# Kernel tuning notes

Hardware: AMD Instinct MI355X
Metric: run time of the kernel (lower is better)

## Reference

```python
import jax, jax.numpy as jnp
import numpy as np

HIDDEN = 4096
MAX_STROKES = 1000
INPUT = 5


def setup_inputs() -> dict:
    key = jax.random.key(0)
    ks = jax.random.split(key, 7)
    s = 1.0 / np.sqrt(HIDDEN)  # torch LSTMCell init scale
    return {
        "W_ih": jax.random.normal(ks[0], (4 * HIDDEN, INPUT), jnp.float32) * s,
        "W_hh": jax.random.normal(ks[1], (4 * HIDDEN, HIDDEN), jnp.float32) * s,
        "b_ih": jax.random.normal(ks[2], (4 * HIDDEN,), jnp.float32) * s,
        "b_hh": jax.random.normal(ks[3], (4 * HIDDEN,), jnp.float32) * s,
        "W_lin": jax.random.normal(ks[4], (7, HIDDEN), jnp.float32) * s,
        "b_lin": jax.random.normal(ks[5], (7,), jnp.float32) * s,
        "noise": jax.random.normal(ks[6], (MAX_STROKES, 2), jnp.float32),
    }


def reference(W_ih, W_hh, b_ih, b_hh, W_lin, b_lin, noise):
    # carried state, so h = c = 0 every step; W_hh @ h vanishes.
    init = jnp.array([0.0, 0.0, 1.0, 0.0, 0.0], dtype=W_ih.dtype)
    mu_idx = jnp.array([0, 2])
    lv_idx = jnp.array([1, 3])

    def step(carry, n_t):
        prev, active = carry  # prev: [5], active: bool (loop condition on prev)
        gates = W_ih @ prev + b_ih + b_hh  # [4H]; W_hh @ 0 omitted
        i_g, f_g, g_g, o_g = jnp.split(gates, 4)
        c = jax.nn.sigmoid(i_g) * jnp.tanh(g_g)
        h = jax.nn.sigmoid(o_g) * jnp.tanh(c)
        logits = jnp.tanh(W_lin @ h + b_lin)  # [7]
        pen = jax.nn.softmax(logits[4:])  # [3]
        xy = logits[mu_idx] + jnp.exp(logits[lv_idx] / 2.0) * n_t  # reparam sample
        new_row = jnp.concatenate([xy, pen])  # [5]
        row_out = jnp.where(active, new_row, 0.0)
        next_prev = jnp.where(active, new_row, prev)
        next_active = jnp.logical_and(active, jnp.argmax(new_row[2:]) != 2)
        return (next_prev, next_active), row_out

    (_, _), rows = jax.lax.scan(step, (init, jnp.array(True)), noise)
    return jnp.concatenate([init[None, :], rows], axis=0)  # [MAX_STROKES+1, 5]
```

## Files before the change

kernel.cpp:

```cpp
#include <hip/hip_runtime.h>
#include <math.h>

#define H 4096
#define NSTEPS 1000
#define NT 512
#define NGATEBLK 12
#define NWLBLK 7
#define NREPACK (NGATEBLK + NWLBLK)
#define MAGIC 0x5A17C0DEull

typedef float f32x2 __attribute__((ext_vector_type(2)));


__device__ __forceinline__ unsigned short f2bf(float f) {
    unsigned u = __builtin_bit_cast(unsigned, f);
    u += 0x7FFFu + ((u >> 16) & 1u);
    return (unsigned short)(u >> 16);
}
__device__ __forceinline__ float bf2f(unsigned h) {
    unsigned u = h << 16;
    return __builtin_bit_cast(float, u);
}
__device__ __forceinline__ unsigned long long pack4(float a, float b, float c, float d) {
    return (unsigned long long)f2bf(a) | ((unsigned long long)f2bf(b) << 16)
         | ((unsigned long long)f2bf(c) << 32) | ((unsigned long long)f2bf(d) << 48);
}
__device__ __forceinline__ unsigned pack2(float a, float b) {
    return (unsigned)f2bf(a) | ((unsigned)f2bf(b) << 16);
}

__device__ __forceinline__ f32x2 sig3(f32x2 z) {
    f32x2 z2 = z * z;
    f32x2 p = z2 * (-1.0f / 48.0f) + 0.25f;
    return z * p + 0.5f;
}
__device__ __forceinline__ f32x2 tanh7(f32x2 z) {
    f32x2 z2 = z * z;
    f32x2 p = z2 * (-0.0539682540f) + 0.1333333333f;
    p = z2 * p + (-0.3333333333f);
    return (z * z2) * p + z;
}
__device__ __forceinline__ f32x2 tanh3(f32x2 z) {
    f32x2 z2 = z * z;
    f32x2 p = z2 * (-0.3333333333f) + 1.0f;
    return z * p;
}
__device__ __forceinline__ float poly_tanh(float z) {
    float z2 = z * z;
    float p = fmaf(z2, -0.0539682540f, 0.1333333333f);
    p = fmaf(z2, p, -0.3333333333f);
    return fmaf(z * z2, p, z);
}
__device__ __forceinline__ float poly_exp(float z) {
    float p = fmaf(z, 0.0083333333f, 0.0416666667f);
    p = fmaf(z, p, 0.1666666667f);
    p = fmaf(z, p, 0.5f);
    p = fmaf(z, p, 1.0f);
    return fmaf(z, p, 1.0f);
}

__global__ __launch_bounds__(NT, 1) void sketch_fused(
    const float* __restrict__ W_ih,
    const float* __restrict__ b_ih,
    const float* __restrict__ b_hh,
    const float* __restrict__ W_lin,
    const float* __restrict__ b_lin,
    const float* __restrict__ noise,
    float* __restrict__ out,
    unsigned char* __restrict__ ws)
{
    unsigned long long* ws8 = (unsigned long long*)ws;
    unsigned* wsu = (unsigned*)(ws + (size_t)38 * 512 * 8);
    unsigned long long* flags = (unsigned long long*)(ws + (512u << 10));
    const int tid = threadIdx.x;
    const int blk = blockIdx.x;

    if (blk < NREPACK) {
        if (blk < NGATEBLK) {
            const int g = blk >> 2, p = blk & 3;
            const int up = p * 512 + tid;
            const int s  = up >> 2;
            const int j  = up & 3;
            const size_t f2w = (g == 0) ? 0 : (g == 1 ? (size_t)5 * H : (size_t)15 * H / 2);
            const float2* Wf2 = (const float2*)W_ih;
            float2 A  = Wf2[f2w + 5 * (size_t)up + 0];
            float2 Bv = Wf2[f2w + 5 * (size_t)up + 1];
            float2 Cc = Wf2[f2w + 5 * (size_t)up + 2];
            float2 D  = Wf2[f2w + 5 * (size_t)up + 3];
            float2 E  = Wf2[f2w + 5 * (size_t)up + 4];
            const size_t f2b = (g == 0) ? 0 : (g == 1 ? (size_t)H : (size_t)3 * H / 2);
            float2 bi = ((const float2*)b_ih)[f2b + up];
            float2 bh = ((const float2*)b_hh)[f2b + up];
            float b0 = bi.x + bh.x + Cc.x;
            float b1 = bi.y + bh.y + E.y;
            unsigned long long wA = pack4(A.x, Cc.y, A.y, D.x);
            unsigned long long wB = pack4(Bv.x - Cc.x, D.y - E.y, Bv.y - Cc.x, E.x - E.y);
            const int rA = g * 8 + 2 * j;
            __hip_atomic_store(&ws8[(size_t)rA * 512 + s],       wA, __ATOMIC_RELAXED, __HIP_MEMORY_SCOPE_AGENT);
            __hip_atomic_store(&ws8[(size_t)(rA + 1) * 512 + s], wB, __ATOMIC_RELAXED, __HIP_MEMORY_SCOPE_AGENT);
            __hip_atomic_store(&wsu[(size_t)(g * 4 + j) * 512 + s], pack2(b0, b1),
                               __ATOMIC_RELAXED, __HIP_MEMORY_SCOPE_AGENT);
        } else {
            const int l = blk - NGATEBLK;
            const float4* p4 = (const float4*)(W_lin + (size_t)l * H);
            float4 v0 = p4[2 * tid], v1 = p4[2 * tid + 1];
            unsigned long long wA = pack4(v0.x, v0.y, v0.z, v0.w);
            unsigned long long wB = pack4(v1.x, v1.y, v1.z, v1.w);
            __hip_atomic_store(&ws8[(size_t)(24 + 2 * l) * 512 + tid], wA, __ATOMIC_RELAXED, __HIP_MEMORY_SCOPE_AGENT);
            __hip_atomic_store(&ws8[(size_t)(25 + 2 * l) * 512 + tid], wB, __ATOMIC_RELAXED, __HIP_MEMORY_SCOPE_AGENT);
        }
        asm volatile("s_waitcnt vmcnt(0)" ::: "memory");
        __syncthreads();
        if (tid == 0)
            __hip_atomic_store(&flags[blk], MAGIC, __ATOMIC_RELAXED, __HIP_MEMORY_SCOPE_AGENT);
        return;
    }

    const int lane = tid & 63;
    const int wave = tid >> 6;

    __shared__ __align__(16) float s_noise[NSTEPS * 2];
    __shared__ float s_part[8][8];
    __shared__ float s_prev[8];

    if (tid < 500)
        ((float4*)s_noise)[tid] = ((const float4*)noise)[tid];

    for (int i = tid; i < (NSTEPS + 1) * 5; i += NT) out[i] = (i == 2) ? 1.f : 0.f;

    if (wave == 0 && lane < NREPACK) {
        int guard = 0;
        while (__hip_atomic_load(&flags[lane], __ATOMIC_RELAXED, __HIP_MEMORY_SCOPE_AGENT) != MAGIC) {
            __builtin_amdgcn_s_sleep(2);
            if (++guard > (1 << 26)) break;
        }
    }
    __syncthreads();

    f32x2 Wg[3][4][4];
    f32x2 Bg[3][4];
    f32x2 WL[7][4];
    {
        unsigned long long raw[19];
#pragma unroll
        for (int r = 0; r < 19; ++r)
            raw[r] = __hip_atomic_load(&ws8[(size_t)r * 512 + tid], __ATOMIC_RELAXED, __HIP_MEMORY_SCOPE_AGENT);
#pragma unroll
        for (int r = 0; r < 19; ++r) {
            unsigned lo = (unsigned)raw[r], hi = (unsigned)(raw[r] >> 32);
            f32x2 e01 = {bf2f(lo & 0xFFFFu), bf2f(lo >> 16)};
            f32x2 e23 = {bf2f(hi & 0xFFFFu), bf2f(hi >> 16)};
            const int g = r >> 3, j = (r & 7) >> 1, isB = r & 1;
            Wg[g][isB ? 2 : 0][j] = e01;
            Wg[g][isB ? 3 : 1][j] = e23;
        }
#pragma unroll
        for (int r = 19; r < 38; ++r)
            raw[r - 19] = __hip_atomic_load(&ws8[(size_t)r * 512 + tid], __ATOMIC_RELAXED, __HIP_MEMORY_SCOPE_AGENT);
#pragma unroll
        for (int r = 19; r < 38; ++r) {
            unsigned lo = (unsigned)raw[r - 19], hi = (unsigned)(raw[r - 19] >> 32);
            f32x2 e01 = {bf2f(lo & 0xFFFFu), bf2f(lo >> 16)};
            f32x2 e23 = {bf2f(hi & 0xFFFFu), bf2f(hi >> 16)};
            if (r < 24) {
                const int g = r >> 3, j = (r & 7) >> 1, isB = r & 1;
                Wg[g][isB ? 2 : 0][j] = e01;
                Wg[g][isB ? 3 : 1][j] = e23;
            } else {
                const int m = r - 24, l = m >> 1, h = m & 1;
                WL[l][2 * h]     = e01;
                WL[l][2 * h + 1] = e23;
            }
        }
        unsigned rawb[12];
#pragma unroll
        for (int r = 0; r < 12; ++r)
            rawb[r] = __hip_atomic_load(&wsu[(size_t)r * 512 + tid], __ATOMIC_RELAXED, __HIP_MEMORY_SCOPE_AGENT);
#pragma unroll
        for (int r = 0; r < 12; ++r) {
            f32x2 e = {bf2f(rawb[r] & 0xFFFFu), bf2f(rawb[r] >> 16)};
            Bg[r >> 2][r & 3] = e;
        }
    }
    const float blin = (lane < 7 && wave == 0) ? b_lin[lane] : 0.f;

    float pv0 = 0.f, pv1 = 0.f, pv2 = 1.f, pv3 = 0.f;

    for (int t = 0; t < NSTEPS; ++t) {
        const f32x2 P0 = {pv0, pv0}, P1 = {pv1, pv1}, P2 = {pv2, pv2}, P3 = {pv3, pv3};
        f32x2 AC0 = {0.f, 0.f}, AC1 = AC0, AC2 = AC0, AC3 = AC0, AC4 = AC0, AC5 = AC0, AC6 = AC0;
#pragma unroll
        for (int j = 0; j < 4; ++j) {
            f32x2 gi = Wg[0][0][j] * P0 + Bg[0][j];
            gi = Wg[0][1][j] * P1 + gi;
            gi = Wg[0][2][j] * P2 + gi;
            gi = Wg[0][3][j] * P3 + gi;
            f32x2 gg = Wg[1][0][j] * P0 + Bg[1][j];
            gg = Wg[1][1][j] * P1 + gg;
            gg = Wg[1][2][j] * P2 + gg;
            gg = Wg[1][3][j] * P3 + gg;
            f32x2 go = Wg[2][0][j] * P0 + Bg[2][j];
            go = Wg[2][1][j] * P1 + go;
            go = Wg[2][2][j] * P2 + go;
            go = Wg[2][3][j] * P3 + go;
            f32x2 c = sig3(gi) * tanh7(gg);
            f32x2 h = sig3(go) * tanh3(c);
            AC0 = WL[0][j] * h + AC0;
            AC1 = WL[1][j] * h + AC1;
            AC2 = WL[2][j] * h + AC2;
            AC3 = WL[3][j] * h + AC3;
            AC4 = WL[4][j] * h + AC4;
            AC5 = WL[5][j] * h + AC5;
            AC6 = WL[6][j] * h + AC6;
        }
        float a0 = AC0.x + AC0.y, a1 = AC1.x + AC1.y, a2 = AC2.x + AC2.y;
        float a3 = AC3.x + AC3.y, a4 = AC4.x + AC4.y, a5 = AC5.x + AC5.y;
        float a6 = AC6.x + AC6.y;
#pragma unroll
        for (int m = 1; m < 64; m <<= 1) {
            a0 += __shfl_xor(a0, m, 64);
            a1 += __shfl_xor(a1, m, 64);
            a2 += __shfl_xor(a2, m, 64);
            a3 += __shfl_xor(a3, m, 64);
            a4 += __shfl_xor(a4, m, 64);
            a5 += __shfl_xor(a5, m, 64);
            a6 += __shfl_xor(a6, m, 64);
        }
        if (lane == 0) {
            s_part[wave][0] = a0; s_part[wave][1] = a1; s_part[wave][2] = a2;
            s_part[wave][3] = a3; s_part[wave][4] = a4; s_part[wave][5] = a5;
            s_part[wave][6] = a6;
        }
        __syncthreads();
        if (wave == 0) {
            const int l = lane < 7 ? lane : 0;
            float s = blin;
#pragma unroll
            for (int w = 0; w < 8; ++w) s += s_part[w][l];
            float lg = poly_tanh(s);
            float l0 = __shfl(lg, 0, 64), l1 = __shfl(lg, 1, 64), l2 = __shfl(lg, 2, 64);
            float l3 = __shfl(lg, 3, 64), l4 = __shfl(lg, 4, 64), l5 = __shfl(lg, 5, 64);
            float l6 = __shfl(lg, 6, 64);
            if (lane == 0) {
                float mx = fmaxf(l4, fmaxf(l5, l6));
                float e0 = poly_exp(l4 - mx), e1 = poly_exp(l5 - mx), e2 = poly_exp(l6 - mx);
                float inv = __fdividef(1.f, e0 + e1 + e2);
                float p0 = e0 * inv, p1 = e1 * inv, p2 = e2 * inv;
                float x0 = fmaf(poly_exp(l1 * 0.5f), s_noise[2 * t],     l0);
                float x1 = fmaf(poly_exp(l3 * 0.5f), s_noise[2 * t + 1], l2);
                float* row = out + (t + 1) * 5;
                row[0] = x0; row[1] = x1; row[2] = p0; row[3] = p1; row[4] = p2;
                s_prev[0] = x0; s_prev[1] = x1; s_prev[2] = p0; s_prev[3] = p1;
                s_prev[5] = (e2 > e0 && e2 > e1) ? 1.f : 0.f;
            }
        }
        __syncthreads();
        pv0 = s_prev[0]; pv1 = s_prev[1]; pv2 = s_prev[2]; pv3 = s_prev[3];
        if (s_prev[5] != 0.f) break;
    }
}

extern "C" void kernel_launch(void* const* d_in, const int* in_sizes, int n_in,
                              void* d_out, int out_size, void* d_ws, size_t ws_size,
                              hipStream_t stream) {
    const float* W_ih  = (const float*)d_in[0];
    const float* b_ih  = (const float*)d_in[2];
    const float* b_hh  = (const float*)d_in[3];
    const float* W_lin = (const float*)d_in[4];
    const float* b_lin = (const float*)d_in[5];
    const float* noise = (const float*)d_in[6];
    float* out = (float*)d_out;

    hipLaunchKernelGGL(sketch_fused, dim3(NREPACK + 1), dim3(NT), 0, stream,
                       W_ih, b_ih, b_hh, W_lin, b_lin, noise, out,
                       (unsigned char*)d_ws);
}
```

Measured before the change: 19.10 us.

## Replace serial reduction and second barrier with redundant per-wave epilogue

The per-step cross-lane reduction now packs the seven accumulators into shared shuffle stages (transpose-style merge), so each wave issues fewer shuffles. Partials go to a double-buffered shared array. Every wave then reduces the 8x7 partials and computes the tanh/softmax/sample epilogue redundantly, which removes the second __syncthreads and the shared-memory broadcast of the previous row. The output initialisation also switches to float4 stores. The cost is duplicated scalar epilogue work in every wave and reliance on bitwise-identical results across waves so the break stays uniform.

```diff
diff --git a/kernel.cpp b/kernel.cpp
--- a/kernel.cpp
+++ b/kernel.cpp
@@ -57,6 +57,16 @@
     p = fmaf(z, p, 0.5f);
     p = fmaf(z, p, 1.0f);
     return fmaf(z, p, 1.0f);
+}
+
+__device__ __forceinline__ float mergep(float aE, float aO, int lane, int m) {
+    float u = (lane & m) ? aE : aO;
+    float w = __shfl_xor(u, m, 64);
+    float base = (lane & m) ? aO : aE;
+    return base + w;
+}
+__device__ __forceinline__ float rdlane(float v, int l) {
+    return __builtin_bit_cast(float, __builtin_amdgcn_readlane(__builtin_bit_cast(int, v), l));
 }
 
 __global__ __launch_bounds__(NT, 1) void sketch_fused(
@@ -120,13 +130,18 @@
     const int wave = tid >> 6;
 
     __shared__ __align__(16) float s_noise[NSTEPS * 2];
-    __shared__ float s_part[8][8];
-    __shared__ float s_prev[8];
+    __shared__ float s_part[2][8][8];
 
     if (tid < 500)
         ((float4*)s_noise)[tid] = ((const float4*)noise)[tid];
-
-    for (int i = tid; i < (NSTEPS + 1) * 5; i += NT) out[i] = (i == 2) ? 1.f : 0.f;
+    if (tid < 16) s_part[tid & 1][tid >> 1][7] = 0.f;
+
+    {
+        float4* o4 = (float4*)out;
+        for (int i = tid; i < 1251; i += NT)
+            o4[i] = (i == 0) ? make_float4(0.f, 0.f, 1.f, 0.f) : make_float4(0.f, 0.f, 0.f, 0.f);
+        if (tid == 0) out[5004] = 0.f;
+    }
 
     if (wave == 0 && lane < NREPACK) {
         int guard = 0;
@@ -182,7 +197,8 @@
             Bg[r >> 2][r & 3] = e;
         }
     }
-    const float blin = (lane < 7 && wave == 0) ? b_lin[lane] : 0.f;
+    const float bl0 = b_lin[0], bl1 = b_lin[1], bl2 = b_lin[2], bl3 = b_lin[3];
+    const float bl4 = b_lin[4], bl5 = b_lin[5], bl6 = b_lin[6];
 
     float pv0 = 0.f, pv1 = 0.f, pv2 = 1.f, pv3 = 0.f;
 
@@ -216,47 +232,45 @@
         float a0 = AC0.x + AC0.y, a1 = AC1.x + AC1.y, a2 = AC2.x + AC2.y;
         float a3 = AC3.x + AC3.y, a4 = AC4.x + AC4.y, a5 = AC5.x + AC5.y;
         float a6 = AC6.x + AC6.y;
-#pragma unroll
-        for (int m = 1; m < 64; m <<= 1) {
-            a0 += __shfl_xor(a0, m, 64);
-            a1 += __shfl_xor(a1, m, 64);
-            a2 += __shfl_xor(a2, m, 64);
-            a3 += __shfl_xor(a3, m, 64);
-            a4 += __shfl_xor(a4, m, 64);
-            a5 += __shfl_xor(a5, m, 64);
-            a6 += __shfl_xor(a6, m, 64);
-        }
-        if (lane == 0) {
-            s_part[wave][0] = a0; s_part[wave][1] = a1; s_part[wave][2] = a2;
-            s_part[wave][3] = a3; s_part[wave][4] = a4; s_part[wave][5] = a5;
-            s_part[wave][6] = a6;
-        }
+
+        float r01 = mergep(a0, a1, lane, 1);
+        float r23 = mergep(a2, a3, lane, 1);
+        float r45 = mergep(a4, a5, lane, 1);
+        float r66 = a6 + __shfl_xor(a6, 1, 64);
+        float r03 = mergep(r01, r23, lane, 2);
+        float r46 = mergep(r45, r66, lane, 2);
+        float rr  = mergep(r03, r46, lane, 4);
+        rr += __shfl_xor(rr, 8, 64);
+        rr += __shfl_xor(rr, 16, 64);
+        rr += __shfl_xor(rr, 32, 64);
+
+        const int lb = t & 1;
+        if (lane < 7) s_part[lb][wave][lane] = rr;
         __syncthreads();
-        if (wave == 0) {
-            const int l = lane < 7 ? lane : 0;
-            float s = blin;
-#pragma unroll
-            for (int w = 0; w < 8; ++w) s += s_part[w][l];
-            float lg = poly_tanh(s);
-            float l0 = __shfl(lg, 0, 64), l1 = __shfl(lg, 1, 64), l2 = __shfl(lg, 2, 64);
-            float l3 = __shfl(lg, 3, 64), l4 = __shfl(lg, 4, 64), l5 = __shfl(lg, 5, 64);
-            float l6 = __shfl(lg, 6, 64);
-            if (lane == 0) {
-                float mx = fmaxf(l4, fmaxf(l5, l6));
-                float e0 = poly_exp(l4 - mx), e1 = poly_exp(l5 - mx), e2 = poly_exp(l6 - mx);
-                float inv = __fdividef(1.f, e0 + e1 + e2);
-                float p0 = e0 * inv, p1 = e1 * inv, p2 = e2 * inv;
-                float x0 = fmaf(poly_exp(l1 * 0.5f), s_noise[2 * t],     l0);
-                float x1 = fmaf(poly_exp(l3 * 0.5f), s_noise[2 * t + 1], l2);
-                float* row = out + (t + 1) * 5;
-                row[0] = x0; row[1] = x1; row[2] = p0; row[3] = p1; row[4] = p2;
-                s_prev[0] = x0; s_prev[1] = x1; s_prev[2] = p0; s_prev[3] = p1;
-                s_prev[5] = (e2 > e0 && e2 > e1) ? 1.f : 0.f;
-            }
-        }
-        __syncthreads();
-        pv0 = s_prev[0]; pv1 = s_prev[1]; pv2 = s_prev[2]; pv3 = s_prev[3];
-        if (s_prev[5] != 0.f) break;
+        float v = s_part[lb][lane >> 3][lane & 7];
+        v += __shfl_xor(v, 8, 64);
+        v += __shfl_xor(v, 16, 64);
+        v += __shfl_xor(v, 32, 64);
+
+        float q0 = poly_tanh(rdlane(v, 0) + bl0);
+        float q1 = poly_tanh(rdlane(v, 1) + bl1);
+        float q2 = poly_tanh(rdlane(v, 2) + bl2);
+        float q3 = poly_tanh(rdlane(v, 3) + bl3);
+        float q4 = poly_tanh(rdlane(v, 4) + bl4);
+        float q5 = poly_tanh(rdlane(v, 5) + bl5);
+        float q6 = poly_tanh(rdlane(v, 6) + bl6);
+        float mx = fmaxf(q4, fmaxf(q5, q6));
+        float e0 = poly_exp(q4 - mx), e1 = poly_exp(q5 - mx), e2 = poly_exp(q6 - mx);
+        float inv = __fdividef(1.f, e0 + e1 + e2);
+        float p0 = e0 * inv, p1 = e1 * inv, p2 = e2 * inv;
+        float x0 = fmaf(poly_exp(q1 * 0.5f), s_noise[2 * t],     q0);
+        float x1 = fmaf(poly_exp(q3 * 0.5f), s_noise[2 * t + 1], q2);
+        if (tid == 0) {
+            float* row = out + (t + 1) * 5;
+            row[0] = x0; row[1] = x1; row[2] = p0; row[3] = p1; row[4] = p2;
+        }
+        pv0 = x0; pv1 = x1; pv2 = p0; pv3 = p1;
+        if (e2 > e0 && e2 > e1) break;
     }
 }
 
```

After: 16.84 us. 1.13x faster.
